# Kernel tuning notes

Measured on AMD Instinct MI355X. Metric: run time of the kernel, lower is better.

The kernel has to match this reference:

```python
import jax, jax.numpy as jnp
import numpy as np

NUM_HEADS = 16
NEG = -1e9


def setup_inputs() -> dict:
    key = jax.random.key(0)
    ks = jax.random.split(key, 9)
    B, S, D = 1, 4096, 1024
    s = 1.0 / np.sqrt(D)
    return {
        "x": jax.random.normal(ks[0], (B, S, D), dtype=jnp.float32),
        "wq": jax.random.normal(ks[1], (D, D), dtype=jnp.float32) * s,
        "bq": jax.random.normal(ks[2], (D,), dtype=jnp.float32) * s,
        "wk": jax.random.normal(ks[3], (D, D), dtype=jnp.float32) * s,
        "bk": jax.random.normal(ks[4], (D,), dtype=jnp.float32) * s,
        "wv": jax.random.normal(ks[5], (D, D), dtype=jnp.float32) * s,
        "bv": jax.random.normal(ks[6], (D,), dtype=jnp.float32) * s,
        "wo": jax.random.normal(ks[7], (D, D), dtype=jnp.float32) * s,
        "bo": jax.random.normal(ks[8], (D,), dtype=jnp.float32) * s,
    }


def reference(x, wq, bq, wk, bk, wv, bv, wo, bo):
    B, S, D = x.shape
    H = NUM_HEADS
    hs = D // H
    # torch Linear: y = x @ W^T + b
    q = x @ wq.T + bq
    k = x @ wk.T + bk
    v = x @ wv.T + bv
    # [B, S, D] -> [B, H, S, hs]
    q = q.reshape(B, S, H, hs).transpose(0, 2, 1, 3)
    k = k.reshape(B, S, H, hs).transpose(0, 2, 1, 3)
    v = v.reshape(B, S, H, hs).transpose(0, 2, 1, 3)
    scores = jnp.einsum("bhqd,bhkd->bhqk", q, k) / jnp.sqrt(jnp.asarray(hs, x.dtype))
    causal = jnp.tril(jnp.ones((S, S), dtype=bool))  # True = keep
    scores = jnp.where(causal, scores, jnp.asarray(NEG, x.dtype))
    weights = jax.nn.softmax(scores, axis=-1)
    out = jnp.einsum("bhqk,bhkd->bhqd", weights, v)
    out = out.transpose(0, 2, 1, 3).reshape(B, S, D)
    return out @ wo.T + bo
```

## Files before the change

kernel.cpp:

```cpp
#include <hip/hip_runtime.h>

#define SEQ 4096
#define DM  1024
#define NH  16
#define HS  64
#define LDQK 2048

typedef __attribute__((ext_vector_type(8))) _Float16 f16x8;
typedef __attribute__((ext_vector_type(4))) _Float16 f16x4;
typedef __attribute__((ext_vector_type(4))) float    f32x4;

#define MFMA16(a, b, c) __builtin_amdgcn_mfma_f32_16x16x32_f16((a), (b), (c), 0, 0, 0)

#define AS1(p) ((const __attribute__((address_space(1))) void*)(p))
#define AS3(p) ((__attribute__((address_space(3))) void*)(p))

#define DPP_ROR_F(x, N) __int_as_float(__builtin_amdgcn_update_dpp( \
    0, __float_as_int(x), 0x120 + (N), 0xF, 0xF, false))

__device__ __forceinline__ float red16_add(float x) {
    x += DPP_ROR_F(x, 1);
    x += DPP_ROR_F(x, 2);
    x += DPP_ROR_F(x, 4);
    x += DPP_ROR_F(x, 8);
    return x;
}

__global__ __launch_bounds__(256) void cast_all(
    const float* __restrict__ x,
    const float* __restrict__ wq, const float* __restrict__ wk,
    const float* __restrict__ wv, const float* __restrict__ wo,
    _Float16* __restrict__ xb, _Float16* __restrict__ wqkb,
    _Float16* __restrict__ wvb, _Float16* __restrict__ wob)
{
    const float* s; _Float16* d; int i;
    if (blockIdx.y == 0) {
        s = x; d = xb;
        i = blockIdx.x * 1024 + threadIdx.x * 4;
    } else {
        int wsel = blockIdx.x >> 10;
        int bx   = blockIdx.x & 1023;
        switch (wsel) {
            case 0:  s = wq; d = wqkb;               break;
            case 1:  s = wk; d = wqkb + (1u << 20);  break;
            case 2:  s = wv; d = wvb;                break;
            default: s = wo; d = wob;                break;
        }
        i = bx * 1024 + threadIdx.x * 4;
    }
    float4 v = *reinterpret_cast<const float4*>(s + i);
    f16x4 o = {(_Float16)v.x, (_Float16)v.y, (_Float16)v.z, (_Float16)v.w};
    *reinterpret_cast<f16x4*>(d + i) = o;
}

template <int BM, typename OUT_T>
__device__ __forceinline__ void gemm_core(
    const _Float16* __restrict__ A,
    const _Float16* __restrict__ W,
    const float*    __restrict__ bias,
    int nbase, int bias_row,
    OUT_T* __restrict__ C,
    int N, int K, float scale, int m0, int n0,
    _Float16* As_, _Float16* Bs_)
{
    constexpr int MI = BM / 32;

    const int t    = threadIdx.x;
    const int w    = t >> 6;
    const int lane = t & 63;
    const int q    = lane >> 4;
    const int l    = lane & 15;
    const int wm   = (w & 1) * (BM / 2);
    const int wn   = (w >> 1) * 64;

    const int srow = lane >> 3;
    const int scol = ((lane & 7) ^ (lane >> 3)) * 8;

    auto stage = [&](int p, int k0) {
        #pragma unroll
        for (int j = 0; j < BM / 32; ++j) {
            int c = w * (BM / 32) + j;
            __builtin_amdgcn_global_load_lds(
                AS1(A + (size_t)(m0 + c * 8 + srow) * K + k0 + scol),
                AS3((char*)As_ + p * (BM * 128) + c * 1024), 16, 0, 0);
        }
        #pragma unroll
        for (int j = 0; j < 4; ++j) {
            int c = w * 4 + j;
            __builtin_amdgcn_global_load_lds(
                AS1(W + (size_t)(n0 + c * 8 + srow) * K + k0 + scol),
                AS3((char*)Bs_ + p * 16384 + c * 1024), 16, 0, 0);
        }
    };

    f32x4 acc[MI][4];
    #pragma unroll
    for (int i = 0; i < MI; ++i)
        #pragma unroll
        for (int j = 0; j < 4; ++j) acc[i][j] = (f32x4){0.f, 0.f, 0.f, 0.f};

    stage(0, 0);
    int p = 0;
    for (int k0 = 0; k0 < K; k0 += 64) {
        __syncthreads();
        if (k0 + 64 < K) stage(p ^ 1, k0 + 64);

        #pragma unroll
        for (int ks = 0; ks < 64; ks += 32) {
            f16x8 af[MI], bf[4];
            #pragma unroll
            for (int i = 0; i < MI; ++i) {
                int r = wm + i * 16 + l;
                af[i] = *reinterpret_cast<const f16x8*>(
                    (const char*)As_ + p * (BM * 128) + r * 128 +
                    ((((ks >> 3) + q) ^ (l & 7)) << 4));
            }
            #pragma unroll
            for (int j = 0; j < 4; ++j) {
                int r = wn + j * 16 + l;
                bf[j] = *reinterpret_cast<const f16x8*>(
                    (const char*)Bs_ + p * 16384 + r * 128 +
                    ((((ks >> 3) + q) ^ (l & 7)) << 4));
            }
            #pragma unroll
            for (int i = 0; i < MI; ++i)
                #pragma unroll
                for (int j = 0; j < 4; ++j)
                    acc[i][j] = MFMA16(af[i], bf[j], acc[i][j]);
        }
        p ^= 1;
    }

    #pragma unroll
    for (int i = 0; i < MI; ++i) {
        #pragma unroll
        for (int j = 0; j < 4; ++j) {
            int gnb = n0 + wn + j * 16 + l;
            float bc2 = bias_row ? 0.f : bias[gnb - nbase];
            #pragma unroll
            for (int r = 0; r < 4; ++r) {
                int gm = m0 + wm + i * 16 + q * 4 + r;
                float bb = bias_row ? bias[gm] : bc2;
                C[(size_t)gm * N + gnb] = (OUT_T)((acc[i][j][r] + bb) * scale);
            }
        }
    }
}

__global__ __launch_bounds__(256, 2) void gemm_qkv(
    const _Float16* __restrict__ xb, const _Float16* __restrict__ wqkb,
    const _Float16* __restrict__ wvb,
    const float* __restrict__ bq, const float* __restrict__ bk,
    const float* __restrict__ bv,
    _Float16* __restrict__ QKb, _Float16* __restrict__ Vtb)
{
    __shared__ _Float16 As[2][128][64];
    __shared__ _Float16 Bs[2][128][64];

    const int bid = blockIdx.x;
    if (bid < 512) {
        const int n0 = (bid & 15) * 128, m0 = (bid >> 4) * 128;
        const float* bias = (n0 < 1024) ? bq : bk;
        const int   nbase = (n0 < 1024) ? 0 : 1024;
        const float scale = (n0 < 1024) ? 0.18033688011112042f : 1.0f;
        gemm_core<128, _Float16>(xb, wqkb, bias, nbase, 0, QKb,
                                 2048, 1024, scale, m0, n0,
                                 &As[0][0][0], &Bs[0][0][0]);
    } else {
        const int v = bid - 512;
        const int n0 = (v & 31) * 128, m0 = (v >> 5) * 128;
        gemm_core<128, _Float16>(wvb, xb, bv, 0, 1, Vtb,
                                 4096, 1024, 1.0f, m0, n0,
                                 &As[0][0][0], &Bs[0][0][0]);
    }
}

__global__ __launch_bounds__(256, 2) void gemm_o(
    const _Float16* __restrict__ Ab, const _Float16* __restrict__ wob,
    const float* __restrict__ bo, float* __restrict__ out)
{
    __shared__ _Float16 As[2][64][64];
    __shared__ _Float16 Bs[2][128][64];
    const int n0 = blockIdx.x * 128, m0 = blockIdx.y * 64;
    gemm_core<64, float>(Ab, wob, bo, 0, 0, out, 1024, 1024, 1.0f, m0, n0,
                         &As[0][0][0], &Bs[0][0][0]);
}

#define APAD 72

__global__ __launch_bounds__(256, 4) void attn_mfma(
    const _Float16* __restrict__ Qg,
    const _Float16* __restrict__ Kg,
    const _Float16* __restrict__ Vt,
    _Float16* __restrict__ O)
{
    __shared__ _Float16 Qs[64][APAD];
    __shared__ _Float16 Ks[4][16][APAD];
    __shared__ _Float16 Vs[64][APAD];
    __shared__ _Float16 Ps[64][APAD];

    const int t    = threadIdx.x;
    const int h    = blockIdx.x;
    const int by   = blockIdx.y;
    const int qb   = (by < 32) ? by : 95 - by;
    const int w    = t >> 6;
    const int lane = t & 63;
    const int q    = lane >> 4;
    const int l    = lane & 15;
    const int sr   = t >> 3;
    const int sc   = (t & 7) * 8;
    const int kj   = sr & 3;
    const int kn   = sr >> 2;

    *reinterpret_cast<uint4*>(&Qs[sr][sc]) =
        *reinterpret_cast<const uint4*>(Qg + (size_t)(qb * 64 + sr) * LDQK + h * 64 + sc);
    *reinterpret_cast<uint4*>(&Qs[sr + 32][sc]) =
        *reinterpret_cast<const uint4*>(Qg + (size_t)(qb * 64 + sr + 32) * LDQK + h * 64 + sc);

    uint4 kr0 = *reinterpret_cast<const uint4*>(Kg + (size_t)(sr) * LDQK + h * 64 + sc);
    uint4 kr1 = *reinterpret_cast<const uint4*>(Kg + (size_t)(sr + 32) * LDQK + h * 64 + sc);
    uint4 vr0 = *reinterpret_cast<const uint4*>(Vt + (size_t)(h * 64 + sr) * SEQ + sc);
    uint4 vr1 = *reinterpret_cast<const uint4*>(Vt + (size_t)(h * 64 + sr + 32) * SEQ + sc);

    float l_acc[4] = {0.f, 0.f, 0.f, 0.f};
    f32x4 oacc[4];
    #pragma unroll
    for (int nt = 0; nt < 4; ++nt) oacc[nt] = (f32x4){0.f, 0.f, 0.f, 0.f};

    __syncthreads();
    f16x8 aq0 = *reinterpret_cast<const f16x8*>(&Qs[w * 16 + l][q * 8]);
    f16x8 aq1 = *reinterpret_cast<const f16x8*>(&Qs[w * 16 + l][32 + q * 8]);

    const int qrow_base = qb * 64 + w * 16 + q * 4;

    for (int kt = 0; kt <= qb; ++kt) {
        __syncthreads();
        *reinterpret_cast<uint4*>(&Ks[kj][kn][sc])     = kr0;
        *reinterpret_cast<uint4*>(&Ks[kj][kn + 8][sc]) = kr1;
        *reinterpret_cast<uint4*>(&Vs[sr][sc])         = vr0;
        *reinterpret_cast<uint4*>(&Vs[sr + 32][sc])    = vr1;
        if (kt < qb) {
            kr0 = *reinterpret_cast<const uint4*>(
                Kg + (size_t)((kt + 1) * 64 + sr) * LDQK + h * 64 + sc);
            kr1 = *reinterpret_cast<const uint4*>(
                Kg + (size_t)((kt + 1) * 64 + sr + 32) * LDQK + h * 64 + sc);
            vr0 = *reinterpret_cast<const uint4*>(
                Vt + (size_t)(h * 64 + sr) * SEQ + (kt + 1) * 64 + sc);
            vr1 = *reinterpret_cast<const uint4*>(
                Vt + (size_t)(h * 64 + sr + 32) * SEQ + (kt + 1) * 64 + sc);
        }
        __syncthreads();

        f32x4 s[4];
        __builtin_amdgcn_s_setprio(1);
        #pragma unroll
        for (int jt = 0; jt < 4; ++jt) {
            f16x8 bk0 = *reinterpret_cast<const f16x8*>(&Ks[jt][l][q * 8]);
            f16x8 bk1 = *reinterpret_cast<const f16x8*>(&Ks[jt][l][32 + q * 8]);
            f32x4 z = (f32x4){0.f, 0.f, 0.f, 0.f};
            z = MFMA16(aq0, bk0, z);
            z = MFMA16(aq1, bk1, z);
            s[jt] = z;
        }
        __builtin_amdgcn_s_setprio(0);

        const bool diag = (kt == qb);

        #pragma unroll
        for (int r = 0; r < 4; ++r) {
            float p0 = s[0][r], p1 = s[1][r], p2 = s[2][r], p3 = s[3][r];
            if (diag) {
                const int qg = qrow_base + r;
                const int kg = kt * 64 + 4 * l;
                p0 = (kg + 0 <= qg) ? p0 : -1e30f;
                p1 = (kg + 1 <= qg) ? p1 : -1e30f;
                p2 = (kg + 2 <= qg) ? p2 : -1e30f;
                p3 = (kg + 3 <= qg) ? p3 : -1e30f;
            }
            p0 = __builtin_amdgcn_exp2f(p0 - 4.f);
            p1 = __builtin_amdgcn_exp2f(p1 - 4.f);
            p2 = __builtin_amdgcn_exp2f(p2 - 4.f);
            p3 = __builtin_amdgcn_exp2f(p3 - 4.f);
            l_acc[r] += (p0 + p1) + (p2 + p3);
            f16x4 pk = {(_Float16)p0, (_Float16)p1, (_Float16)p2, (_Float16)p3};
            *reinterpret_cast<f16x4*>(&Ps[w * 16 + q * 4 + r][4 * l]) = pk;
        }

        f16x8 ap0 = *reinterpret_cast<const f16x8*>(&Ps[w * 16 + l][q * 8]);
        f16x8 ap1 = *reinterpret_cast<const f16x8*>(&Ps[w * 16 + l][32 + q * 8]);
        __builtin_amdgcn_s_setprio(1);
        #pragma unroll
        for (int nt = 0; nt < 4; ++nt) {
            f16x8 bv0 = *reinterpret_cast<const f16x8*>(&Vs[nt * 16 + l][q * 8]);
            f16x8 bv1 = *reinterpret_cast<const f16x8*>(&Vs[nt * 16 + l][32 + q * 8]);
            oacc[nt] = MFMA16(ap0, bv0, oacc[nt]);
            oacc[nt] = MFMA16(ap1, bv1, oacc[nt]);
        }
        __builtin_amdgcn_s_setprio(0);
    }

    #pragma unroll
    for (int r = 0; r < 4; ++r) {
        float inv = 1.f / red16_add(l_acc[r]);
        size_t row = (size_t)(qb * 64 + w * 16 + q * 4 + r) * DM + h * 64;
        #pragma unroll
        for (int nt = 0; nt < 4; ++nt)
            O[row + nt * 16 + l] = (_Float16)(oacc[nt][r] * inv);
    }
}

extern "C" void kernel_launch(void* const* d_in, const int* in_sizes, int n_in,
                              void* d_out, int out_size, void* d_ws, size_t ws_size,
                              hipStream_t stream)
{
    const float* x  = (const float*)d_in[0];
    const float* wq = (const float*)d_in[1];
    const float* bq = (const float*)d_in[2];
    const float* wk = (const float*)d_in[3];
    const float* bk = (const float*)d_in[4];
    const float* wv = (const float*)d_in[5];
    const float* bv = (const float*)d_in[6];
    const float* wo = (const float*)d_in[7];
    const float* bo = (const float*)d_in[8];
    float* out = (float*)d_out;

    char* ws = (char*)d_ws;
    _Float16* xb   = (_Float16*)(ws);
    _Float16* wqkb = (_Float16*)(ws + (8ull  << 20));
    _Float16* wvb  = (_Float16*)(ws + (12ull << 20));
    _Float16* wob  = (_Float16*)(ws + (14ull << 20));
    _Float16* QKb  = (_Float16*)(ws + (16ull << 20));
    _Float16* Vtb  = (_Float16*)(ws + (32ull << 20));
    _Float16* Ab   = (_Float16*)(ws + (40ull << 20));

    cast_all<<<dim3(SEQ * DM / 1024, 2), dim3(256), 0, stream>>>(
        x, wq, wk, wv, wo, xb, wqkb, wvb, wob);

    gemm_qkv<<<dim3(768), dim3(256), 0, stream>>>(
        xb, wqkb, wvb, bq, bk, bv, QKb, Vtb);

    attn_mfma<<<dim3(NH, 64), dim3(256), 0, stream>>>(QKb, QKb + 1024, Vtb, Ab);

    gemm_o<<<dim3(DM / 128, SEQ / 64), dim3(256), 0, stream>>>(
        Ab, wob, bo, out);
}
```

Baseline: 211.9 us.

## Drop GEMM LDS double buffering for higher occupancy and XCD-aware block remap

The GEMM core moves from a double-buffered LDS pipeline to a single buffer with a sync before and after each tile load. This halves shared memory per block so launch bounds can rise from 2 to 4 blocks per CU, relying on more resident waves to hide load latency. The QKV GEMM also remaps block indices so that consecutive blocks dispatched to each of the 8 XCDs cover contiguous tiles, aiming for better L2 reuse. The cost is that loads no longer overlap compute within a block, and the extra barrier may stall if occupancy does not actually increase.

```diff
diff --git a/kernel.cpp b/kernel.cpp
--- a/kernel.cpp
+++ b/kernel.cpp
@@ -76,34 +76,29 @@
     const int srow = lane >> 3;
     const int scol = ((lane & 7) ^ (lane >> 3)) * 8;
 
-    auto stage = [&](int p, int k0) {
+    f32x4 acc[MI][4];
+    #pragma unroll
+    for (int i = 0; i < MI; ++i)
+        #pragma unroll
+        for (int j = 0; j < 4; ++j) acc[i][j] = (f32x4){0.f, 0.f, 0.f, 0.f};
+
+    for (int k0 = 0; k0 < K; k0 += 64) {
+        __syncthreads();
         #pragma unroll
         for (int j = 0; j < BM / 32; ++j) {
             int c = w * (BM / 32) + j;
             __builtin_amdgcn_global_load_lds(
                 AS1(A + (size_t)(m0 + c * 8 + srow) * K + k0 + scol),
-                AS3((char*)As_ + p * (BM * 128) + c * 1024), 16, 0, 0);
+                AS3((char*)As_ + c * 1024), 16, 0, 0);
         }
         #pragma unroll
         for (int j = 0; j < 4; ++j) {
             int c = w * 4 + j;
             __builtin_amdgcn_global_load_lds(
                 AS1(W + (size_t)(n0 + c * 8 + srow) * K + k0 + scol),
-                AS3((char*)Bs_ + p * 16384 + c * 1024), 16, 0, 0);
-        }
-    };
-
-    f32x4 acc[MI][4];
-    #pragma unroll
-    for (int i = 0; i < MI; ++i)
-        #pragma unroll
-        for (int j = 0; j < 4; ++j) acc[i][j] = (f32x4){0.f, 0.f, 0.f, 0.f};
-
-    stage(0, 0);
-    int p = 0;
-    for (int k0 = 0; k0 < K; k0 += 64) {
+                AS3((char*)Bs_ + c * 1024), 16, 0, 0);
+        }
         __syncthreads();
-        if (k0 + 64 < K) stage(p ^ 1, k0 + 64);
 
         #pragma unroll
         for (int ks = 0; ks < 64; ks += 32) {
@@ -112,14 +107,14 @@
             for (int i = 0; i < MI; ++i) {
                 int r = wm + i * 16 + l;
                 af[i] = *reinterpret_cast<const f16x8*>(
-                    (const char*)As_ + p * (BM * 128) + r * 128 +
+                    (const char*)As_ + r * 128 +
                     ((((ks >> 3) + q) ^ (l & 7)) << 4));
             }
             #pragma unroll
             for (int j = 0; j < 4; ++j) {
                 int r = wn + j * 16 + l;
                 bf[j] = *reinterpret_cast<const f16x8*>(
-                    (const char*)Bs_ + p * 16384 + r * 128 +
+                    (const char*)Bs_ + r * 128 +
                     ((((ks >> 3) + q) ^ (l & 7)) << 4));
             }
             #pragma unroll
@@ -128,7 +123,6 @@
                 for (int j = 0; j < 4; ++j)
                     acc[i][j] = MFMA16(af[i], bf[j], acc[i][j]);
         }
-        p ^= 1;
     }
 
     #pragma unroll
@@ -147,17 +141,17 @@
     }
 }
 
-__global__ __launch_bounds__(256, 2) void gemm_qkv(
+__global__ __launch_bounds__(256, 4) void gemm_qkv(
     const _Float16* __restrict__ xb, const _Float16* __restrict__ wqkb,
     const _Float16* __restrict__ wvb,
     const float* __restrict__ bq, const float* __restrict__ bk,
     const float* __restrict__ bv,
     _Float16* __restrict__ QKb, _Float16* __restrict__ Vtb)
 {
-    __shared__ _Float16 As[2][128][64];
-    __shared__ _Float16 Bs[2][128][64];
-
-    const int bid = blockIdx.x;
+    __shared__ _Float16 As[128][64];
+    __shared__ _Float16 Bs[128][64];
+
+    const int bid = (blockIdx.x & 7) * 96 + (blockIdx.x >> 3);
     if (bid < 512) {
         const int n0 = (bid & 15) * 128, m0 = (bid >> 4) * 128;
         const float* bias = (n0 < 1024) ? bq : bk;
@@ -165,25 +159,25 @@
         const float scale = (n0 < 1024) ? 0.18033688011112042f : 1.0f;
         gemm_core<128, _Float16>(xb, wqkb, bias, nbase, 0, QKb,
                                  2048, 1024, scale, m0, n0,
-                                 &As[0][0][0], &Bs[0][0][0]);
+                                 &As[0][0], &Bs[0][0]);
     } else {
         const int v = bid - 512;
         const int n0 = (v & 31) * 128, m0 = (v >> 5) * 128;
         gemm_core<128, _Float16>(wvb, xb, bv, 0, 1, Vtb,
                                  4096, 1024, 1.0f, m0, n0,
-                                 &As[0][0][0], &Bs[0][0][0]);
-    }
-}
-
-__global__ __launch_bounds__(256, 2) void gemm_o(
+                                 &As[0][0], &Bs[0][0]);
+    }
+}
+
+__global__ __launch_bounds__(256, 4) void gemm_o(
     const _Float16* __restrict__ Ab, const _Float16* __restrict__ wob,
     const float* __restrict__ bo, float* __restrict__ out)
 {
-    __shared__ _Float16 As[2][64][64];
-    __shared__ _Float16 Bs[2][128][64];
+    __shared__ _Float16 As[64][64];
+    __shared__ _Float16 Bs[128][64];
     const int n0 = blockIdx.x * 128, m0 = blockIdx.y * 64;
     gemm_core<64, float>(Ab, wob, bo, 0, 0, out, 1024, 1024, 1.0f, m0, n0,
-                         &As[0][0][0], &Bs[0][0][0]);
+                         &As[0][0], &Bs[0][0]);
 }
 
 #define APAD 72
```

New measurement: 205.0 us (median of 2 runs). -3.2%, faster.
